# Performance work log

Hardware: AMD Instinct MI355X
Metric: run time of the kernel (lower is better)

The kernel has to match this reference:

```python
import jax, jax.numpy as jnp
import numpy as np

B, N, D, H, DEPTH = 2, 2048, 768, 12, 4
DH = D // H
SCALE = DH ** -0.5
EPS = 1e-5
FF = 4 * D


def layer_norm(x, w, b):
    m = jnp.mean(x, axis=-1, keepdims=True)
    v = jnp.mean((x - m) ** 2, axis=-1, keepdims=True)
    return (x - m) * jax.lax.rsqrt(v + EPS) * w + b


def to_heads(t):  # [b, n, D] -> [b, H, n, DH]
    b, n, _ = t.shape
    return t.reshape(b, n, H, DH).transpose(0, 2, 1, 3)


def merge_heads(t):  # [b, H, n, DH] -> [b, n, D]
    b, h, n, dh = t.shape
    return t.transpose(0, 2, 1, 3).reshape(b, n, D)


def attend(q, k, v, bias):
    s = jnp.einsum('bhid,bhjd->bhij', q, k) * SCALE + bias
    a = jax.nn.softmax(s, axis=-1)
    return merge_heads(jnp.einsum('bhij,bhjd->bhid', a, v))


def setup_inputs():
    key = jax.random.key(0)
    ks = iter(jax.random.split(key, 16))

    def p(shape, scale=0.02):
        return jax.random.normal(next(ks), shape, dtype=jnp.float32) * scale

    inp = {
        'x': jax.random.normal(next(ks), (B, N, D), dtype=jnp.float32),
        'context': jax.random.normal(next(ks), (B, N, D), dtype=jnp.float32),
        'relative_position_bias': jax.random.normal(next(ks), (1, H, N, N), dtype=jnp.float32) * 0.02,
        # self-attn params (stacked over depth)
        'ln1_w': jnp.ones((DEPTH, D), jnp.float32), 'ln1_b': jnp.zeros((DEPTH, D), jnp.float32),
        'w_qkv': p((DEPTH, D, 3 * D)),
        'w_so': p((DEPTH, D, D)), 'b_so': jnp.zeros((DEPTH, D), jnp.float32),
        # cross-attn params (shared LN applied to x and context, as in source)
        'ln2_w': jnp.ones((DEPTH, D), jnp.float32), 'ln2_b': jnp.zeros((DEPTH, D), jnp.float32),
        'w_q': p((DEPTH, D, D)), 'w_k': p((DEPTH, D, D)), 'w_v': p((DEPTH, D, D)),
        'w_co': p((DEPTH, D, D)), 'b_co': jnp.zeros((DEPTH, D), jnp.float32),
        # FFN params
        'ln3_w': jnp.ones((DEPTH, D), jnp.float32), 'ln3_b': jnp.zeros((DEPTH, D), jnp.float32),
        'w_f1': p((DEPTH, D, FF)), 'b_f1': jnp.zeros((DEPTH, FF), jnp.float32),
        'w_f2': p((DEPTH, FF, D)), 'b_f2': jnp.zeros((DEPTH, D), jnp.float32),
        # final norm
        'lnout_w': jnp.ones((D,), jnp.float32), 'lnout_b': jnp.zeros((D,), jnp.float32),
    }
    return inp


def reference(x, context, relative_position_bias,
              ln1_w, ln1_b, w_qkv, w_so, b_so,
              ln2_w, ln2_b, w_q, w_k, w_v, w_co, b_co,
              ln3_w, ln3_b, w_f1, b_f1, w_f2, b_f2,
              lnout_w, lnout_b):
    bias = relative_position_bias
    for i in range(DEPTH):
        # self-attention block (pre-norm, residual)
        xn = layer_norm(x, ln1_w[i], ln1_b[i])
        q, k, v = jnp.split(xn @ w_qkv[i], 3, axis=-1)
        o = attend(to_heads(q), to_heads(k), to_heads(v), bias)
        x = o @ w_so[i] + b_so[i] + x
        # cross-attention block (input_norm shared for x and context)
        xn = layer_norm(x, ln2_w[i], ln2_b[i])
        cn = layer_norm(context, ln2_w[i], ln2_b[i])
        o = attend(to_heads(xn @ w_q[i]), to_heads(cn @ w_k[i]), to_heads(cn @ w_v[i]), bias)
        x = o @ w_co[i] + b_co[i] + x
        # FFN block
        xn = layer_norm(x, ln3_w[i], ln3_b[i])
        h = jax.nn.gelu(xn @ w_f1[i] + b_f1[i], approximate=False)
        x = h @ w_f2[i] + b_f2[i] + x
    return layer_norm(x, lnout_w, lnout_b)
```

## Files before the change

kernel.cpp:

```cpp
#include <hip/hip_runtime.h>
#include <cstdint>
#include <cstddef>

#define DEV static __device__ __forceinline__

typedef float  f32x4 __attribute__((ext_vector_type(4)));
typedef float  f32x2 __attribute__((ext_vector_type(2)));
typedef short  s16x8 __attribute__((ext_vector_type(8)));
typedef unsigned short u16;
typedef unsigned int   u32;
typedef unsigned int   u32x4 __attribute__((ext_vector_type(4)));
typedef unsigned short u16x2 __attribute__((ext_vector_type(2)));
typedef unsigned short u16x4 __attribute__((ext_vector_type(4)));
typedef __bf16 bf16x8 __attribute__((ext_vector_type(8)));

#define LOG2E 1.4426950408889634f
#define QSCALE_CONST 0.18033688011112042f
#define BSCALE 256.0f
#define BINV   0.00390625f

DEV u16 f2bf(float f){ return __builtin_bit_cast(u16, (__bf16)f); }
DEV float bf2f(u16 v){ union { unsigned u; float f; } x; x.u = ((unsigned)v) << 16; return x.f; }

DEV float fexp2(float x){
#if __has_builtin(__builtin_amdgcn_exp2f)
  return __builtin_amdgcn_exp2f(x);
#else
  return exp2f(x);
#endif
}

DEV f32x4 mfma16(s16x8 a, s16x8 b, f32x4 c){
  return __builtin_amdgcn_mfma_f32_16x16x32_bf16(
      __builtin_bit_cast(bf16x8, a), __builtin_bit_cast(bf16x8, b), c, 0, 0, 0);
}

DEV void gld16(const void* g, void* l){
  __builtin_amdgcn_global_load_lds(
      (const __attribute__((address_space(1))) void*)(uintptr_t)g,
      (__attribute__((address_space(3))) void*)(unsigned)(uintptr_t)l,
      16, 0, 0);
}

#if __has_builtin(__builtin_amdgcn_cvt_pk_fp8_f32) && __has_builtin(__builtin_amdgcn_cvt_pk_f32_fp8)
DEV u32 pk4_fp8(f32x4 v){
  int r = __builtin_amdgcn_cvt_pk_fp8_f32(v[0], v[1], 0, false);
  r     = __builtin_amdgcn_cvt_pk_fp8_f32(v[2], v[3], r, true);
  return (u32)r;
}
template<bool HI>
DEV f32x2 upk_fp8(u32 w){
  return __builtin_amdgcn_cvt_pk_f32_fp8((int)w, HI);
}
#else
DEV unsigned enc1(float x){
  union{float f; unsigned u;} c; c.f = x;
  unsigned s = (c.u >> 24) & 0x80;
  int e = (int)((c.u >> 23) & 0xff) - 127;
  unsigned m = c.u & 0x7fffff;
  if (e >= -6){
    unsigned mant = m >> 20, rem = m & 0xfffff;
    if (rem > 0x80000 || (rem == 0x80000 && (mant & 1))) mant++;
    unsigned eb = (unsigned)(e + 7);
    if (mant == 8){ mant = 0; eb++; }
    if (eb >= 16){ eb = 15; mant = 6; }
    return s | (eb << 3) | mant;
  }
  if (e < -10) return s;
  int sh = -6 - e;
  unsigned full = (1u << 23) | m;
  unsigned mant = full >> (20 + sh);
  unsigned rem  = full & ((1u << (20 + sh)) - 1);
  unsigned half = 1u << (19 + sh);
  if (rem > half || (rem == half && (mant & 1))) mant++;
  if (mant == 8) return s | (1u << 3);
  return s | mant;
}
DEV u32 pk4_fp8(f32x4 v){
  return enc1(v[0]) | (enc1(v[1]) << 8) | (enc1(v[2]) << 16) | (enc1(v[3]) << 24);
}
DEV float dec1(unsigned b){
  int s = (b >> 7) & 1, e = (b >> 3) & 15; float m = (float)(b & 7) * 0.125f;
  float v = e ? ldexpf(1.0f + m, e - 7) : ldexpf(m, -6);
  return s ? -v : v;
}
template<bool HI>
DEV f32x2 upk_fp8(u32 w){
  unsigned lo = HI ? ((w >> 16) & 0xff) : (w & 0xff);
  unsigned h2 = HI ? ((w >> 24) & 0xff) : ((w >> 8) & 0xff);
  f32x2 r; r[0] = dec1(lo); r[1] = dec1(h2); return r;
}
#endif

__global__ void __launch_bounds__(256)
transpose_cvt(const float* __restrict__ src, u16* __restrict__ dst, int K, int N,
              size_t dzstride){
  int z = blockIdx.z;
  src += (size_t)z * K * N;
  dst += (size_t)z * dzstride;
  __shared__ float t[32][33];
  int n0 = blockIdx.x * 32, k0 = blockIdx.y * 32;
#pragma unroll
  for (int i = 0; i < 4; ++i)
    t[threadIdx.y + 8*i][threadIdx.x] = src[(size_t)(k0 + threadIdx.y + 8*i) * N + n0 + threadIdx.x];
  __syncthreads();
#pragma unroll
  for (int i = 0; i < 4; ++i)
    dst[(size_t)(n0 + threadIdx.y + 8*i) * K + k0 + threadIdx.x] = f2bf(t[threadIdx.x][threadIdx.y + 8*i]);
}

struct TPtrs { const float* src[20]; u16* dst[20]; };
__global__ void __launch_bounds__(256)
transpose_cvt_batch(TPtrs tp){
  const float* src = tp.src[blockIdx.z];
  u16* dst = tp.dst[blockIdx.z];
  __shared__ float t[32][33];
  int n0 = blockIdx.x * 32, k0 = blockIdx.y * 32;
#pragma unroll
  for (int i = 0; i < 4; ++i)
    t[threadIdx.y + 8*i][threadIdx.x] = src[(size_t)(k0 + threadIdx.y + 8*i) * 768 + n0 + threadIdx.x];
  __syncthreads();
#pragma unroll
  for (int i = 0; i < 4; ++i)
    dst[(size_t)(n0 + threadIdx.y + 8*i) * 768 + k0 + threadIdx.x] = f2bf(t[threadIdx.x][threadIdx.y + 8*i]);
}

__global__ void __launch_bounds__(256)
cvt_biasT(const float* __restrict__ in, unsigned char* __restrict__ out){
  const int kvt = blockIdx.x, qt = blockIdx.y, h = blockIdx.z, tid = threadIdx.x;
  const int q  = qt * 64 + ((tid >> 6) << 4) + (tid & 15);
  const int c0 = kvt * 64 + ((tid >> 4) & 3) * 4;
  const float* src = in + ((size_t)h * 2048 + q) * 2048;
  u32x4 wv;
#pragma unroll
  for (int mi = 0; mi < 4; ++mi){
    f32x4 v = *(const f32x4*)(src + c0 + mi * 16);
#pragma unroll
    for (int r = 0; r < 4; ++r) v[r] = fminf(fmaxf(v[r] * (LOG2E * BSCALE), -448.f), 448.f);
    wv[mi] = pk4_fp8(v);
  }
  *(u32x4*)(out + ((size_t)(h * 32 + qt) * 32 + kvt) * 4096 + tid * 16) = wv;
}

__global__ void __launch_bounds__(256)
lnv(const float* __restrict__ x, const float* __restrict__ w, const float* __restrict__ b,
    u16* __restrict__ out){
  const int wv = threadIdx.x >> 6, lane = threadIdx.x & 63;
  const float* wz = w + blockIdx.y * 768;
  const float* bz = b + blockIdx.y * 768;
  out += (size_t)blockIdx.y * 4096 * 768;
  const int row = blockIdx.x * 4 + wv;
  const float* xr = x + (size_t)row * 768;
  f32x4 t[3]; float s = 0.f, s2 = 0.f;
#pragma unroll
  for (int c = 0; c < 3; ++c){
    t[c] = *(const f32x4*)(xr + c * 256 + lane * 4);
#pragma unroll
    for (int j = 0; j < 4; ++j){ s += t[c][j]; s2 += t[c][j] * t[c][j]; }
  }
#pragma unroll
  for (int off = 1; off < 64; off <<= 1){ s += __shfl_xor(s, off); s2 += __shfl_xor(s2, off); }
  float m = s * (1.f/768.f);
  float rstd = rsqrtf(s2 * (1.f/768.f) - m * m + 1e-5f);
#pragma unroll
  for (int c = 0; c < 3; ++c){
    const int col = c * 256 + lane * 4;
    f32x4 wv4 = *(const f32x4*)(wz + col);
    f32x4 bv4 = *(const f32x4*)(bz + col);
    u16x4 o;
#pragma unroll
    for (int j = 0; j < 4; ++j) o[j] = f2bf((t[c][j] - m) * rstd * wv4[j] + bv4[j]);
    *(u16x4*)(out + (size_t)row * 768 + col) = o;
  }
}

__global__ void __launch_bounds__(256)
ln_init(const float* __restrict__ x, const float* __restrict__ w, const float* __restrict__ b,
        u16* __restrict__ xn, u16* __restrict__ xbuf){
  const int wv = threadIdx.x >> 6, lane = threadIdx.x & 63;
  const int row = blockIdx.x * 4 + wv;
  const float* xr = x + (size_t)row * 768;
  f32x4 t[3]; float s = 0.f, s2 = 0.f;
#pragma unroll
  for (int c = 0; c < 3; ++c){
    t[c] = *(const f32x4*)(xr + c * 256 + lane * 4);
#pragma unroll
    for (int j = 0; j < 4; ++j){ s += t[c][j]; s2 += t[c][j] * t[c][j]; }
  }
#pragma unroll
  for (int off = 1; off < 64; off <<= 1){ s += __shfl_xor(s, off); s2 += __shfl_xor(s2, off); }
  float m = s * (1.f/768.f);
  float rstd = rsqrtf(s2 * (1.f/768.f) - m * m + 1e-5f);
#pragma unroll
  for (int c = 0; c < 3; ++c){
    const int col = c * 256 + lane * 4;
    f32x4 wv4 = *(const f32x4*)(w + col);
    f32x4 bv4 = *(const f32x4*)(b + col);
    u16x4 o, xb;
#pragma unroll
    for (int j = 0; j < 4; ++j){
      o[j]  = f2bf((t[c][j] - m) * rstd * wv4[j] + bv4[j]);
      xb[j] = f2bf(t[c][j]);
    }
    *(u16x4*)(xn   + (size_t)row * 768 + col) = o;
    *(u16x4*)(xbuf + (size_t)row * 768 + col) = xb;
  }
}

template<typename OUT, int NZ>
__global__ void __launch_bounds__(256)
red_ln(const u16* __restrict__ pb, const float* __restrict__ biasrow,
       u16* __restrict__ xbuf, OUT* __restrict__ out,
       const float* __restrict__ lw, const float* __restrict__ lb){
  const int wv = threadIdx.x >> 6, lane = threadIdx.x & 63;
  const int row = blockIdx.x * 4 + wv;
  const size_t S = 4096ll * 768;
  const u16* p0 = pb + (size_t)row * 768;
  u16* xr = xbuf + (size_t)row * 768;
  f32x4 t[3]; float s = 0.f, s2 = 0.f;
#pragma unroll
  for (int c = 0; c < 3; ++c){
    const int col = c * 256 + lane * 4;
    f32x4 v = *(const f32x4*)(biasrow + col);
    u16x4 xv = *(const u16x4*)(xr + col);
#pragma unroll
    for (int j = 0; j < 4; ++j) v[j] += bf2f(xv[j]);
#pragma unroll
    for (int z = 0; z < NZ; ++z){
      u16x4 pv = *(const u16x4*)(p0 + z * S + col);
#pragma unroll
      for (int j = 0; j < 4; ++j) v[j] += bf2f(pv[j]);
    }
    u16x4 xo;
#pragma unroll
    for (int j = 0; j < 4; ++j) xo[j] = f2bf(v[j]);
    *(u16x4*)(xr + col) = xo;
    t[c] = v;
#pragma unroll
    for (int j = 0; j < 4; ++j){ s += v[j]; s2 += v[j] * v[j]; }
  }
#pragma unroll
  for (int off = 1; off < 64; off <<= 1){ s += __shfl_xor(s, off); s2 += __shfl_xor(s2, off); }
  float m = s * (1.f/768.f);
  float rstd = rsqrtf(s2 * (1.f/768.f) - m * m + 1e-5f);
#pragma unroll
  for (int c = 0; c < 3; ++c){
    const int col = c * 256 + lane * 4;
    f32x4 wv4 = *(const f32x4*)(lw + col);
    f32x4 bv4 = *(const f32x4*)(lb + col);
    if constexpr (sizeof(OUT) == 2){
      u16x4 o;
#pragma unroll
      for (int j = 0; j < 4; ++j) o[j] = f2bf((t[c][j] - m) * rstd * wv4[j] + bv4[j]);
      *(u16x4*)((u16*)out + (size_t)row * 768 + col) = o;
    } else {
      f32x4 o;
#pragma unroll
      for (int j = 0; j < 4; ++j) o[j] = (t[c][j] - m) * rstd * wv4[j] + bv4[j];
      *(f32x4*)((float*)out + (size_t)row * 768 + col) = o;
    }
  }
}

template<int EPI>
__global__ void __launch_bounds__(256)
gemm_bf16(const u16* __restrict__ A, int lda, const u16* __restrict__ Bt, int ldb,
          int nk, u16* __restrict__ Cb, int ldc,
          const float* __restrict__ bias,
          const u16* __restrict__ A2, const u16* __restrict__ Bt2){
  __shared__ u16 As[2][128 * 32];
  __shared__ u16 Bs[2][128 * 32];
  float colscale = 1.0f;
  if constexpr (EPI == 4){
    const int z = blockIdx.z;
    if (z == 0){ colscale = QSCALE_CONST; }
    else { A = A2; Bt = Bt2 + (size_t)(z - 1) * 768 * 768; }
    Cb += z * 768;
  }
  if constexpr (EPI == 5){
    const int z = blockIdx.z;
    A  += (size_t)z * nk * 32;
    Bt += (size_t)z * nk * 32;
    Cb += (size_t)z * 4096 * 768;
  }
  const int gx = gridDim.x, nwg = gx * gridDim.y;
  int lin = blockIdx.y * gx + blockIdx.x;
  {
    const int qq = nwg >> 3, rr = nwg & 7;
    const int xc = lin & 7, oo = lin >> 3;
    lin = (xc < rr ? xc * (qq + 1) : rr * (qq + 1) + (xc - rr) * qq) + oo;
  }
  const int m0 = (lin % gx) * 128, n0 = (lin / gx) * 128;

  const int tid = threadIdx.x, w = tid >> 6, lane = tid & 63;
  const int l16 = lane & 15, g = lane >> 4;
  const int wm = (w >> 1) * 64, wn = (w & 1) * 64;
  f32x4 acc[4][4] = {};

  const u16* a0 = A  + (size_t)(m0 + (tid >> 2)) * lda + (tid & 3) * 8;
  const u16* a1 = A  + (size_t)(m0 + (tid >> 2) + 64) * lda + (tid & 3) * 8;
  const u16* b0 = Bt + (size_t)(n0 + (tid >> 2)) * ldb + (tid & 3) * 8;
  const u16* b1 = Bt + (size_t)(n0 + (tid >> 2) + 64) * ldb + (tid & 3) * 8;

  {
    char* ab = (char*)As[0]; char* bb = (char*)Bs[0];
    gld16(a0, ab + w * 1024); gld16(a1, ab + 4096 + w * 1024);
    gld16(b0, bb + w * 1024); gld16(b1, bb + 4096 + w * 1024);
  }
  __syncthreads();

  int cb = 0;
  for (int kt = 0; kt < nk; ++kt){
    if (kt + 1 < nk){
      const int k1 = (kt + 1) * 32;
      char* ab = (char*)As[cb ^ 1]; char* bb = (char*)Bs[cb ^ 1];
      gld16(a0 + k1, ab + w * 1024); gld16(a1 + k1, ab + 4096 + w * 1024);
      gld16(b0 + k1, bb + w * 1024); gld16(b1 + k1, bb + 4096 + w * 1024);
    }
    const u16* Ab = As[cb]; const u16* Bb = Bs[cb];
    s16x8 af[4], bfv[4];
#pragma unroll
    for (int mi = 0; mi < 4; ++mi)
      af[mi] = *(const s16x8*)(Ab + (wm + mi*16 + l16) * 32 + 8 * g);
#pragma unroll
    for (int ni = 0; ni < 4; ++ni)
      bfv[ni] = *(const s16x8*)(Bb + (wn + ni*16 + l16) * 32 + 8 * g);
#pragma unroll
    for (int mi = 0; mi < 4; ++mi)
#pragma unroll
      for (int ni = 0; ni < 4; ++ni)
        acc[mi][ni] = mfma16(af[mi], bfv[ni], acc[mi][ni]);
    __syncthreads();
    cb ^= 1;
  }

#pragma unroll
  for (int mi = 0; mi < 4; ++mi){
    const int rg = m0 + wm + mi*16 + 4*g;
#pragma unroll
    for (int ni = 0; ni < 4; ++ni){
      const int col = n0 + wn + ni*16 + l16;
      f32x4 v = acc[mi][ni];
#pragma unroll
      for (int r = 0; r < 4; ++r){
        const int row = rg + r;
        if constexpr (EPI == 2){
          float t = v[r] + bias[col];
          float ge = 0.5f * t * (1.0f + erff(t * 0.7071067811865476f));
          Cb[(size_t)row * ldc + col] = f2bf(ge);
        } else if constexpr (EPI == 3){
          float sc = (col < 768) ? QSCALE_CONST : 1.0f;
          Cb[(size_t)row * ldc + col] = f2bf(v[r] * sc);
        } else if constexpr (EPI == 4){
          Cb[(size_t)row * ldc + col] = f2bf(v[r] * colscale);
        } else {
          Cb[(size_t)row * 768 + col] = f2bf(v[r]);
        }
      }
    }
  }
}

__global__ void __launch_bounds__(256)
attn_kernel(const u16* __restrict__ qkv, const unsigned char* __restrict__ biasT,
            u16* __restrict__ out){
  __shared__ __align__(16) u16 Ks[2][4096];
  __shared__ __align__(16) u16 Vt[2][4096];
  __shared__ __align__(16) u16 Pl[4][1024];

  const int tid = threadIdx.x, w = tid >> 6, lane = tid & 63;
  const int l16 = lane & 15, g = lane >> 4;
  const int qt = blockIdx.x, h = blockIdx.y, b = blockIdx.z;
  const int rowbase = b * 2048, q0 = qt * 64;

  const int ci0 = w * 64 + lane, ci1 = ci0 + 256;
  const int r0 = ci0 >> 3, sc0 = ci0 & 7, r1 = ci1 >> 3, sc1 = ci1 & 7;
  const u16* kp0 = qkv + (size_t)(rowbase + r0) * 2304 + 768 + h * 64 + (((sc0 ^ (r0 & 7)) & 7) << 3);
  const u16* kp1 = qkv + (size_t)(rowbase + r1) * 2304 + 768 + h * 64 + (((sc1 ^ (r1 & 7)) & 7) << 3);
  const int dh0 = (tid & 31) * 2, vs = tid >> 5;
  const u16* vp = qkv + (size_t)(rowbase + vs * 8) * 2304 + 1536 + h * 64 + dh0;
  u16x2 vr[8];
  const unsigned char* bT = biasT + ((size_t)(h * 32 + qt) * 32) * 4096 + tid * 16;
  u32x4 brW, bnW;

  const u16* qrow = qkv + (size_t)(rowbase + q0 + w * 16 + l16) * 2304 + h * 64;
  s16x8 qf0 = *(const s16x8*)(qrow + 8 * g);
  s16x8 qf1 = *(const s16x8*)(qrow + 32 + 8 * g);

  f32x4 oacc[4] = {};
  float mrun = -3.0e38f, lrun = 0.f;
  const int sw = l16 & 7;

  {
    char* kb = (char*)Ks[0] + w * 1024;
    gld16(kp0, kb); gld16(kp1, kb + 4096);
#pragma unroll
    for (int i = 0; i < 8; ++i) vr[i] = *(const u16x2*)(vp + (size_t)i * 2304);
    brW = *(const u32x4*)(bT);
    s16x8 vA, vB;
#pragma unroll
    for (int j = 0; j < 8; ++j){ vA[j] = (short)vr[j][0]; vB[j] = (short)vr[j][1]; }
    *(s16x8*)(Vt[0] + dh0 * 64 + ((vs ^ (dh0 & 7)) << 3)) = vA;
    *(s16x8*)(Vt[0] + (dh0 + 1) * 64 + ((vs ^ ((dh0 + 1) & 7)) << 3)) = vB;
  }
  __syncthreads();

  for (int t = 0; t < 32; ++t){
    const int cb = t & 1;
    if (t < 31){
      const size_t koff = (size_t)(t + 1) * 64 * 2304;
      char* kb = (char*)Ks[cb ^ 1] + w * 1024;
      gld16(kp0 + koff, kb); gld16(kp1 + koff, kb + 4096);
      const u16* p = vp + koff;
#pragma unroll
      for (int i = 0; i < 8; ++i) vr[i] = *(const u16x2*)(p + (size_t)i * 2304);
      bnW = *(const u32x4*)(bT + (size_t)(t + 1) * 4096);
    }

    f32x4 st[4];
    __builtin_amdgcn_s_setprio(1);
#pragma unroll
    for (int mi = 0; mi < 4; ++mi){
      const int row = l16 + 16 * mi;
      s16x8 kf0 = *(const s16x8*)(Ks[cb] + row * 64 + ((g ^ sw) << 3));
      s16x8 kf1 = *(const s16x8*)(Ks[cb] + row * 64 + (((g + 4) ^ sw) << 3));
      f32x4 z = {};
      z = mfma16(kf0, qf0, z);
      st[mi] = mfma16(kf1, qf1, z);
    }
    __builtin_amdgcn_s_setprio(0);

    float tmax = -3.0e38f;
#pragma unroll
    for (int mi = 0; mi < 4; ++mi){
      f32x2 lo = upk_fp8<false>(brW[mi]);
      f32x2 hi = upk_fp8<true>(brW[mi]);
      st[mi][0] = fmaf(lo[0], BINV, st[mi][0]);
      st[mi][1] = fmaf(lo[1], BINV, st[mi][1]);
      st[mi][2] = fmaf(hi[0], BINV, st[mi][2]);
      st[mi][3] = fmaf(hi[1], BINV, st[mi][3]);
#pragma unroll
      for (int r = 0; r < 4; ++r) tmax = fmaxf(tmax, st[mi][r]);
    }
    tmax = fmaxf(tmax, __shfl_xor(tmax, 16));
    tmax = fmaxf(tmax, __shfl_xor(tmax, 32));
    if (!__all(tmax <= mrun + 8.f)){
      float mnew = fmaxf(mrun, tmax);
      float al = fexp2(mrun - mnew);
      mrun = mnew;
      lrun *= al;
#pragma unroll
      for (int r = 0; r < 4; ++r){
        float aq = __shfl(al, 4 * g + r);
#pragma unroll
        for (int ni = 0; ni < 4; ++ni) oacc[ni][r] *= aq;
      }
    }
    float ssum = 0.f;
#pragma unroll
    for (int mi = 0; mi < 4; ++mi){
      u16x4 pk;
#pragma unroll
      for (int r = 0; r < 4; ++r){
        float pv = fexp2(st[mi][r] - mrun);
        ssum += pv;
        pk[r] = f2bf(pv);
      }
      *(u16x4*)(Pl[w] + l16 * 64 + (((2*mi + (g >> 1)) ^ sw) << 3) + 4 * (g & 1)) = pk;
    }
    ssum += __shfl_xor(ssum, 16);
    ssum += __shfl_xor(ssum, 32);
    lrun += ssum;

    __builtin_amdgcn_s_setprio(1);
#pragma unroll
    for (int ks2 = 0; ks2 < 2; ++ks2){
      s16x8 pf = *(const s16x8*)(Pl[w] + l16 * 64 + (((4*ks2 + g) ^ sw) << 3));
#pragma unroll
      for (int ni = 0; ni < 4; ++ni){
        const int dh = l16 + 16 * ni;
        s16x8 vf = *(const s16x8*)(Vt[cb] + dh * 64 + (((4*ks2 + g) ^ sw) << 3));
        oacc[ni] = mfma16(pf, vf, oacc[ni]);
      }
    }
    __builtin_amdgcn_s_setprio(0);

    if (t < 31){
      s16x8 vA, vB;
#pragma unroll
      for (int j = 0; j < 8; ++j){ vA[j] = (short)vr[j][0]; vB[j] = (short)vr[j][1]; }
      *(s16x8*)(Vt[cb ^ 1] + dh0 * 64 + ((vs ^ (dh0 & 7)) << 3)) = vA;
      *(s16x8*)(Vt[cb ^ 1] + (dh0 + 1) * 64 + ((vs ^ ((dh0 + 1) & 7)) << 3)) = vB;
      brW = bnW;
    }
    __syncthreads();
  }

#pragma unroll
  for (int r = 0; r < 4; ++r){
    float lq = __shfl(lrun, 4 * g + r);
    float inv = 1.0f / lq;
    const int row = rowbase + q0 + w * 16 + 4 * g + r;
#pragma unroll
    for (int ni = 0; ni < 4; ++ni)
      out[(size_t)row * 768 + h * 64 + l16 + 16 * ni] = f2bf(oacc[ni][r] * inv);
  }
}

extern "C" void kernel_launch(void* const* d_in, const int* in_sizes, int n_in,
                              void* d_out, int out_size, void* d_ws, size_t ws_size,
                              hipStream_t stream){
  const float* in_x    = (const float*)d_in[0];
  const float* in_ctx  = (const float*)d_in[1];
  const float* in_bias = (const float*)d_in[2];
  const float* ln1_w = (const float*)d_in[3];
  const float* ln1_b = (const float*)d_in[4];
  const float* w_qkv = (const float*)d_in[5];
  const float* w_so  = (const float*)d_in[6];
  const float* b_so  = (const float*)d_in[7];
  const float* ln2_w = (const float*)d_in[8];
  const float* ln2_b = (const float*)d_in[9];
  const float* w_q   = (const float*)d_in[10];
  const float* w_k   = (const float*)d_in[11];
  const float* w_v   = (const float*)d_in[12];
  const float* w_co  = (const float*)d_in[13];
  const float* b_co  = (const float*)d_in[14];
  const float* ln3_w = (const float*)d_in[15];
  const float* ln3_b = (const float*)d_in[16];
  const float* w_f1  = (const float*)d_in[17];
  const float* b_f1  = (const float*)d_in[18];
  const float* w_f2  = (const float*)d_in[19];
  const float* b_f2  = (const float*)d_in[20];
  const float* lnout_w = (const float*)d_in[21];
  const float* lnout_b = (const float*)d_in[22];

  char* p = (char*)d_ws;
  u16* xbuf    = (u16*)p;    p += 4096ll * 768 * 2;
  u16* pbuf    = (u16*)p;    p += 4ll * 4096 * 768 * 2;
  u16* xn      = (u16*)p;    p += 4096ll * 768 * 2;
  u16* cn      = (u16*)p;    p += 4ll * 4096 * 768 * 2;
  u16* qkvb    = (u16*)p;    p += 4096ll * 2304 * 2;
  u16* attO    = (u16*)p;    p += 4096ll * 768 * 2;
  u16* ffh     = (u16*)p;    p += 4096ll * 3072 * 2;
  u16* wqkvT   = (u16*)p;    p += 4ll * 2304 * 768 * 2;
  u16* wsoT    = (u16*)p;    p += 4ll * 768 * 768 * 2;
  u16* wqT     = (u16*)p;    p += 4ll * 768 * 768 * 2;
  u16* wkvT    = (u16*)p;    p += 4ll * 1536 * 768 * 2;
  u16* wcoT    = (u16*)p;    p += 4ll * 768 * 768 * 2;
  u16* wf1T    = (u16*)p;    p += 4ll * 3072 * 768 * 2;
  u16* wf2T    = (u16*)p;    p += 4ll * 768 * 3072 * 2;
  unsigned char* biasT = (unsigned char*)p; p += 12ll * 2048 * 2048;

  const dim3 tb(32, 8);
  transpose_cvt<<<dim3(72, 24, 4), tb, 0, stream>>>(w_qkv, wqkvT, 768, 2304, 2304ll*768);
  transpose_cvt<<<dim3(96, 24, 4), tb, 0, stream>>>(w_f1,  wf1T,  768, 3072, 3072ll*768);
  transpose_cvt<<<dim3(24, 96, 4), tb, 0, stream>>>(w_f2,  wf2T,  3072, 768, 768ll*3072);
  {
    TPtrs tp;
    for (int i = 0; i < 4; ++i){
      tp.src[i*5+0] = w_so + (size_t)i*768*768;  tp.dst[i*5+0] = wsoT + (size_t)i*768*768;
      tp.src[i*5+1] = w_q  + (size_t)i*768*768;  tp.dst[i*5+1] = wqT  + (size_t)i*768*768;
      tp.src[i*5+2] = w_k  + (size_t)i*768*768;  tp.dst[i*5+2] = wkvT + (size_t)i*1536*768;
      tp.src[i*5+3] = w_v  + (size_t)i*768*768;  tp.dst[i*5+3] = wkvT + (size_t)i*1536*768 + 768ll*768;
      tp.src[i*5+4] = w_co + (size_t)i*768*768;  tp.dst[i*5+4] = wcoT + (size_t)i*768*768;
    }
    transpose_cvt_batch<<<dim3(24, 24, 20), tb, 0, stream>>>(tp);
  }
  cvt_biasT<<<dim3(32, 32, 12), 256, 0, stream>>>(in_bias, biasT);
  lnv<<<dim3(1024, 4), 256, 0, stream>>>(in_ctx, ln2_w, ln2_b, cn);
  ln_init<<<1024, 256, 0, stream>>>(in_x, ln1_w, ln1_b, xn, xbuf);

  const dim3 ag(32, 12, 2);
  for (int i = 0; i < 4; ++i){
    gemm_bf16<3><<<dim3(32, 18), 256, 0, stream>>>(xn, 768, wqkvT + (size_t)i*2304*768, 768, 24,
                                                   qkvb, 2304, nullptr, nullptr, nullptr);
    attn_kernel<<<ag, 256, 0, stream>>>(qkvb, biasT, attO);
    gemm_bf16<5><<<dim3(32, 6, 2), 256, 0, stream>>>(attO, 768, wsoT + (size_t)i*768*768, 768, 12,
                                                     pbuf, 768, nullptr, nullptr, nullptr);
    red_ln<u16,2><<<1024, 256, 0, stream>>>(pbuf, b_so + i*768, xbuf, xn, ln2_w + i*768, ln2_b + i*768);
    gemm_bf16<4><<<dim3(32, 6, 3), 256, 0, stream>>>(xn, 768, wqT + (size_t)i*768*768, 768, 24,
                                                     qkvb, 2304, nullptr,
                                                     cn + (size_t)i*4096*768, wkvT + (size_t)i*1536*768);
    attn_kernel<<<ag, 256, 0, stream>>>(qkvb, biasT, attO);
    gemm_bf16<5><<<dim3(32, 6, 2), 256, 0, stream>>>(attO, 768, wcoT + (size_t)i*768*768, 768, 12,
                                                     pbuf, 768, nullptr, nullptr, nullptr);
    red_ln<u16,2><<<1024, 256, 0, stream>>>(pbuf, b_co + i*768, xbuf, xn, ln3_w + i*768, ln3_b + i*768);
    gemm_bf16<2><<<dim3(32, 24), 256, 0, stream>>>(xn, 768, wf1T + (size_t)i*3072*768, 768, 24,
                                                   ffh, 3072, b_f1 + i*3072, nullptr, nullptr);
    gemm_bf16<5><<<dim3(32, 6, 4), 256, 0, stream>>>(ffh, 3072, wf2T + (size_t)i*768*3072, 3072, 24,
                                                     pbuf, 768, nullptr, nullptr, nullptr);
    if (i < 3)
      red_ln<u16,4><<<1024, 256, 0, stream>>>(pbuf, b_f2 + i*768, xbuf, xn, ln1_w + (i+1)*768, ln1_b + (i+1)*768);
    else
      red_ln<float,4><<<1024, 256, 0, stream>>>(pbuf, b_f2 + i*768, xbuf, (float*)d_out, lnout_w, lnout_b);
  }
}
```

Before: 1.273 ms.

## Merge preprocessing layernorms, process two rows per wave in red_ln, tree max

Merges the context and input layernorm kernels into one launch, where the context rows are read once and normalized for all four depth weights instead of being re-read four times. The residual-reduce layernorm now handles two rows per wave with interleaved shuffle reductions, halving the grid size, to expose more memory-level parallelism. The attention row-max becomes a tree reduction to shorten the dependency chain. These are small pieces of the total runtime, which is dominated by GEMMs and attention.

After: 1.273 ms. No clear change (-0.1%).

```diff
diff --git a/kernel.cpp b/kernel.cpp
--- a/kernel.cpp
+++ b/kernel.cpp
@@ -143,14 +143,13 @@
 }
 
 __global__ void __launch_bounds__(256)
-lnv(const float* __restrict__ x, const float* __restrict__ w, const float* __restrict__ b,
-    u16* __restrict__ out){
+ln_pre(const float* __restrict__ x, const float* __restrict__ ctx,
+       const float* __restrict__ w1, const float* __restrict__ b1,
+       const float* __restrict__ w2, const float* __restrict__ b2,
+       u16* __restrict__ xn, u16* __restrict__ xbuf, u16* __restrict__ cn){
   const int wv = threadIdx.x >> 6, lane = threadIdx.x & 63;
-  const float* wz = w + blockIdx.y * 768;
-  const float* bz = b + blockIdx.y * 768;
-  out += (size_t)blockIdx.y * 4096 * 768;
   const int row = blockIdx.x * 4 + wv;
-  const float* xr = x + (size_t)row * 768;
+  const float* xr = (blockIdx.y == 0 ? x : ctx) + (size_t)row * 768;
   f32x4 t[3]; float s = 0.f, s2 = 0.f;
 #pragma unroll
   for (int c = 0; c < 3; ++c){
@@ -162,48 +161,36 @@
   for (int off = 1; off < 64; off <<= 1){ s += __shfl_xor(s, off); s2 += __shfl_xor(s2, off); }
   float m = s * (1.f/768.f);
   float rstd = rsqrtf(s2 * (1.f/768.f) - m * m + 1e-5f);
-#pragma unroll
-  for (int c = 0; c < 3; ++c){
-    const int col = c * 256 + lane * 4;
-    f32x4 wv4 = *(const f32x4*)(wz + col);
-    f32x4 bv4 = *(const f32x4*)(bz + col);
-    u16x4 o;
-#pragma unroll
-    for (int j = 0; j < 4; ++j) o[j] = f2bf((t[c][j] - m) * rstd * wv4[j] + bv4[j]);
-    *(u16x4*)(out + (size_t)row * 768 + col) = o;
-  }
-}
-
-__global__ void __launch_bounds__(256)
-ln_init(const float* __restrict__ x, const float* __restrict__ w, const float* __restrict__ b,
-        u16* __restrict__ xn, u16* __restrict__ xbuf){
-  const int wv = threadIdx.x >> 6, lane = threadIdx.x & 63;
-  const int row = blockIdx.x * 4 + wv;
-  const float* xr = x + (size_t)row * 768;
-  f32x4 t[3]; float s = 0.f, s2 = 0.f;
-#pragma unroll
-  for (int c = 0; c < 3; ++c){
-    t[c] = *(const f32x4*)(xr + c * 256 + lane * 4);
-#pragma unroll
-    for (int j = 0; j < 4; ++j){ s += t[c][j]; s2 += t[c][j] * t[c][j]; }
-  }
-#pragma unroll
-  for (int off = 1; off < 64; off <<= 1){ s += __shfl_xor(s, off); s2 += __shfl_xor(s2, off); }
-  float m = s * (1.f/768.f);
-  float rstd = rsqrtf(s2 * (1.f/768.f) - m * m + 1e-5f);
-#pragma unroll
-  for (int c = 0; c < 3; ++c){
-    const int col = c * 256 + lane * 4;
-    f32x4 wv4 = *(const f32x4*)(w + col);
-    f32x4 bv4 = *(const f32x4*)(b + col);
-    u16x4 o, xb;
-#pragma unroll
-    for (int j = 0; j < 4; ++j){
-      o[j]  = f2bf((t[c][j] - m) * rstd * wv4[j] + bv4[j]);
-      xb[j] = f2bf(t[c][j]);
-    }
-    *(u16x4*)(xn   + (size_t)row * 768 + col) = o;
-    *(u16x4*)(xbuf + (size_t)row * 768 + col) = xb;
+  if (blockIdx.y == 0){
+#pragma unroll
+    for (int c = 0; c < 3; ++c){
+      const int col = c * 256 + lane * 4;
+      f32x4 wv4 = *(const f32x4*)(w1 + col);
+      f32x4 bv4 = *(const f32x4*)(b1 + col);
+      u16x4 o, xb;
+#pragma unroll
+      for (int j = 0; j < 4; ++j){
+        o[j]  = f2bf((t[c][j] - m) * rstd * wv4[j] + bv4[j]);
+        xb[j] = f2bf(t[c][j]);
+      }
+      *(u16x4*)(xn   + (size_t)row * 768 + col) = o;
+      *(u16x4*)(xbuf + (size_t)row * 768 + col) = xb;
+    }
+  } else {
+#pragma unroll
+    for (int i = 0; i < 4; ++i){
+      u16* dst = cn + (size_t)i * 4096 * 768 + (size_t)row * 768;
+#pragma unroll
+      for (int c = 0; c < 3; ++c){
+        const int col = c * 256 + lane * 4;
+        f32x4 wv4 = *(const f32x4*)(w2 + i * 768 + col);
+        f32x4 bv4 = *(const f32x4*)(b2 + i * 768 + col);
+        u16x4 o;
+#pragma unroll
+        for (int j = 0; j < 4; ++j) o[j] = f2bf((t[c][j] - m) * rstd * wv4[j] + bv4[j]);
+        *(u16x4*)(dst + col) = o;
+      }
+    }
   }
 }
 
@@ -213,51 +200,65 @@
        u16* __restrict__ xbuf, OUT* __restrict__ out,
        const float* __restrict__ lw, const float* __restrict__ lb){
   const int wv = threadIdx.x >> 6, lane = threadIdx.x & 63;
-  const int row = blockIdx.x * 4 + wv;
+  const int row0 = blockIdx.x * 8 + wv * 2;
   const size_t S = 4096ll * 768;
-  const u16* p0 = pb + (size_t)row * 768;
-  u16* xr = xbuf + (size_t)row * 768;
-  f32x4 t[3]; float s = 0.f, s2 = 0.f;
-#pragma unroll
-  for (int c = 0; c < 3; ++c){
-    const int col = c * 256 + lane * 4;
-    f32x4 v = *(const f32x4*)(biasrow + col);
-    u16x4 xv = *(const u16x4*)(xr + col);
-#pragma unroll
-    for (int j = 0; j < 4; ++j) v[j] += bf2f(xv[j]);
-#pragma unroll
-    for (int z = 0; z < NZ; ++z){
-      u16x4 pv = *(const u16x4*)(p0 + z * S + col);
-#pragma unroll
-      for (int j = 0; j < 4; ++j) v[j] += bf2f(pv[j]);
-    }
-    u16x4 xo;
-#pragma unroll
-    for (int j = 0; j < 4; ++j) xo[j] = f2bf(v[j]);
-    *(u16x4*)(xr + col) = xo;
-    t[c] = v;
-#pragma unroll
-    for (int j = 0; j < 4; ++j){ s += v[j]; s2 += v[j] * v[j]; }
-  }
-#pragma unroll
-  for (int off = 1; off < 64; off <<= 1){ s += __shfl_xor(s, off); s2 += __shfl_xor(s2, off); }
-  float m = s * (1.f/768.f);
-  float rstd = rsqrtf(s2 * (1.f/768.f) - m * m + 1e-5f);
-#pragma unroll
-  for (int c = 0; c < 3; ++c){
-    const int col = c * 256 + lane * 4;
-    f32x4 wv4 = *(const f32x4*)(lw + col);
-    f32x4 bv4 = *(const f32x4*)(lb + col);
-    if constexpr (sizeof(OUT) == 2){
-      u16x4 o;
-#pragma unroll
-      for (int j = 0; j < 4; ++j) o[j] = f2bf((t[c][j] - m) * rstd * wv4[j] + bv4[j]);
-      *(u16x4*)((u16*)out + (size_t)row * 768 + col) = o;
-    } else {
-      f32x4 o;
-#pragma unroll
-      for (int j = 0; j < 4; ++j) o[j] = (t[c][j] - m) * rstd * wv4[j] + bv4[j];
-      *(f32x4*)((float*)out + (size_t)row * 768 + col) = o;
+  f32x4 t[2][3]; float s[2] = {0.f, 0.f}, s2[2] = {0.f, 0.f};
+#pragma unroll
+  for (int rr = 0; rr < 2; ++rr){
+    const int row = row0 + rr;
+    const u16* p0 = pb + (size_t)row * 768;
+    u16* xr = xbuf + (size_t)row * 768;
+#pragma unroll
+    for (int c = 0; c < 3; ++c){
+      const int col = c * 256 + lane * 4;
+      f32x4 v = *(const f32x4*)(biasrow + col);
+      u16x4 xv = *(const u16x4*)(xr + col);
+#pragma unroll
+      for (int j = 0; j < 4; ++j) v[j] += bf2f(xv[j]);
+#pragma unroll
+      for (int z = 0; z < NZ; ++z){
+        u16x4 pv = *(const u16x4*)(p0 + z * S + col);
+#pragma unroll
+        for (int j = 0; j < 4; ++j) v[j] += bf2f(pv[j]);
+      }
+      u16x4 xo;
+#pragma unroll
+      for (int j = 0; j < 4; ++j) xo[j] = f2bf(v[j]);
+      *(u16x4*)(xr + col) = xo;
+      t[rr][c] = v;
+#pragma unroll
+      for (int j = 0; j < 4; ++j){ s[rr] += v[j]; s2[rr] += v[j] * v[j]; }
+    }
+  }
+#pragma unroll
+  for (int off = 1; off < 64; off <<= 1){
+#pragma unroll
+    for (int rr = 0; rr < 2; ++rr){
+      s[rr]  += __shfl_xor(s[rr], off);
+      s2[rr] += __shfl_xor(s2[rr], off);
+    }
+  }
+#pragma unroll
+  for (int rr = 0; rr < 2; ++rr){
+    const int row = row0 + rr;
+    float m = s[rr] * (1.f/768.f);
+    float rstd = rsqrtf(s2[rr] * (1.f/768.f) - m * m + 1e-5f);
+#pragma unroll
+    for (int c = 0; c < 3; ++c){
+      const int col = c * 256 + lane * 4;
+      f32x4 wv4 = *(const f32x4*)(lw + col);
+      f32x4 bv4 = *(const f32x4*)(lb + col);
+      if constexpr (sizeof(OUT) == 2){
+        u16x4 o;
+#pragma unroll
+        for (int j = 0; j < 4; ++j) o[j] = f2bf((t[rr][c][j] - m) * rstd * wv4[j] + bv4[j]);
+        *(u16x4*)((u16*)out + (size_t)row * 768 + col) = o;
+      } else {
+        f32x4 o;
+#pragma unroll
+        for (int j = 0; j < 4; ++j) o[j] = (t[rr][c][j] - m) * rstd * wv4[j] + bv4[j];
+        *(f32x4*)((float*)out + (size_t)row * 768 + col) = o;
+      }
     }
   }
 }
@@ -430,7 +431,7 @@
     }
     __builtin_amdgcn_s_setprio(0);
 
-    float tmax = -3.0e38f;
+    float mloc[4];
 #pragma unroll
     for (int mi = 0; mi < 4; ++mi){
       f32x2 lo = upk_fp8<false>(brW[mi]);
@@ -439,9 +440,9 @@
       st[mi][1] = fmaf(lo[1], BINV, st[mi][1]);
       st[mi][2] = fmaf(hi[0], BINV, st[mi][2]);
       st[mi][3] = fmaf(hi[1], BINV, st[mi][3]);
-#pragma unroll
-      for (int r = 0; r < 4; ++r) tmax = fmaxf(tmax, st[mi][r]);
-    }
+      mloc[mi] = fmaxf(fmaxf(st[mi][0], st[mi][1]), fmaxf(st[mi][2], st[mi][3]));
+    }
+    float tmax = fmaxf(fmaxf(mloc[0], mloc[1]), fmaxf(mloc[2], mloc[3]));
     tmax = fmaxf(tmax, __shfl_xor(tmax, 16));
     tmax = fmaxf(tmax, __shfl_xor(tmax, 32));
     if (!__all(tmax <= mrun + 8.f)){
@@ -567,8 +568,8 @@
     transpose_cvt_batch<<<dim3(24, 24, 20), tb, 0, stream>>>(tp);
   }
   cvt_biasT<<<dim3(32, 32, 12), 256, 0, stream>>>(in_bias, biasT);
-  lnv<<<dim3(1024, 4), 256, 0, stream>>>(in_ctx, ln2_w, ln2_b, cn);
-  ln_init<<<1024, 256, 0, stream>>>(in_x, ln1_w, ln1_b, xn, xbuf);
+  ln_pre<<<dim3(1024, 2), 256, 0, stream>>>(in_x, in_ctx, ln1_w, ln1_b, ln2_w, ln2_b,
+                                            xn, xbuf, cn);
 
   const dim3 ag(32, 12, 2);
   for (int i = 0; i < 4; ++i){
@@ -577,21 +578,21 @@
     attn_kernel<<<ag, 256, 0, stream>>>(qkvb, biasT, attO);
     gemm_bf16<5><<<dim3(32, 6, 2), 256, 0, stream>>>(attO, 768, wsoT + (size_t)i*768*768, 768, 12,
                                                      pbuf, 768, nullptr, nullptr, nullptr);
-    red_ln<u16,2><<<1024, 256, 0, stream>>>(pbuf, b_so + i*768, xbuf, xn, ln2_w + i*768, ln2_b + i*768);
+    red_ln<u16,2><<<512, 256, 0, stream>>>(pbuf, b_so + i*768, xbuf, xn, ln2_w + i*768, ln2_b + i*768);
     gemm_bf16<4><<<dim3(32, 6, 3), 256, 0, stream>>>(xn, 768, wqT + (size_t)i*768*768, 768, 24,
                                                      qkvb, 2304, nullptr,
                                                      cn + (size_t)i*4096*768, wkvT + (size_t)i*1536*768);
     attn_kernel<<<ag, 256, 0, stream>>>(qkvb, biasT, attO);
     gemm_bf16<5><<<dim3(32, 6, 2), 256, 0, stream>>>(attO, 768, wcoT + (size_t)i*768*768, 768, 12,
                                                      pbuf, 768, nullptr, nullptr, nullptr);
-    red_ln<u16,2><<<1024, 256, 0, stream>>>(pbuf, b_co + i*768, xbuf, xn, ln3_w + i*768, ln3_b + i*768);
+    red_ln<u16,2><<<512, 256, 0, stream>>>(pbuf, b_co + i*768, xbuf, xn, ln3_w + i*768, ln3_b + i*768);
     gemm_bf16<2><<<dim3(32, 24), 256, 0, stream>>>(xn, 768, wf1T + (size_t)i*3072*768, 768, 24,
                                                    ffh, 3072, b_f1 + i*3072, nullptr, nullptr);
     gemm_bf16<5><<<dim3(32, 6, 4), 256, 0, stream>>>(ffh, 3072, wf2T + (size_t)i*768*3072, 3072, 24,
                                                      pbuf, 768, nullptr, nullptr, nullptr);
     if (i < 3)
-      red_ln<u16,4><<<1024, 256, 0, stream>>>(pbuf, b_f2 + i*768, xbuf, xn, ln1_w + (i+1)*768, ln1_b + (i+1)*768);
+      red_ln<u16,4><<<512, 256, 0, stream>>>(pbuf, b_f2 + i*768, xbuf, xn, ln1_w + (i+1)*768, ln1_b + (i+1)*768);
     else
-      red_ln<float,4><<<1024, 256, 0, stream>>>(pbuf, b_f2 + i*768, xbuf, (float*)d_out, lnout_w, lnout_b);
-  }
-}
+      red_ln<float,4><<<512, 256, 0, stream>>>(pbuf, b_f2 + i*768, xbuf, (float*)d_out, lnout_w, lnout_b);
+  }
+}
```
